# Optimization experiments

Hardware: AMD Instinct MI355X
Metric: run time of the kernel (lower is better)

Reference implementation:

```python
import jax, jax.numpy as jnp
import numpy as np

EPS = 1e-12  # torch F.normalize eps

def _l2norm(v, axis):
    n = jnp.linalg.norm(v, axis=axis, keepdims=True)
    return v / jnp.maximum(n, EPS)

def setup_inputs() -> dict:
    key = jax.random.key(0)
    k1, k2, k3 = jax.random.split(key, 3)
    N, D, H, W, K = 32, 512, 40, 40, 64
    x = jax.random.normal(k1, (N, D, H, W), dtype=jnp.float32)
    conv_weight = jax.random.normal(k2, (K, D), dtype=jnp.float32) * 0.05
    centroids = jax.random.uniform(k3, (K, D), dtype=jnp.float32)
    return {"x": x, "conv_weight": conv_weight, "centroids": centroids}

def reference(x, conv_weight, centroids):
    N, D, H, W = x.shape
    K = centroids.shape[0]
    # descriptor-wise L2 normalization over channel dim
    x = _l2norm(x, axis=1)
    x_flat = x.reshape(N, D, H * W)                       # [N, D, S]
    # 1x1 conv == per-pixel linear: [K,D] @ [N,D,S] -> [N,K,S]
    logits = jnp.einsum('kd,nds->nks', conv_weight, x_flat)
    soft_assign = jax.nn.softmax(logits, axis=1)          # softmax over clusters
    # vlad[n,k,d] = sum_s a[n,k,s] * (x[n,d,s] - c[k,d])
    #            = (a @ x^T) - (sum_s a) * c   -- two GEMM-like ops, no K-loop
    agg = jnp.einsum('nks,nds->nkd', soft_assign, x_flat)  # [N, K, D]
    a_sum = soft_assign.sum(axis=2)                        # [N, K]
    vlad = agg - a_sum[:, :, None] * centroids[None, :, :]
    # intra-normalization over D, flatten, global L2 normalization
    vlad = _l2norm(vlad, axis=2)
    vlad = vlad.reshape(N, K * D)
    vlad = _l2norm(vlad, axis=1)
    return vlad
```

## Files before the change

### kernel.cpp

```cpp
#include <hip/hip_runtime.h>
#include <math.h>

#define N_ 32
#define D_ 512
#define S_ 1600
#define K_ 64

#define APL 72

typedef __attribute__((ext_vector_type(8))) short short8;
typedef __attribute__((ext_vector_type(4))) float f32x4;
typedef __attribute__((ext_vector_type(2))) unsigned u32x2;

static __device__ __forceinline__ short f2bf(float f) {
    unsigned u = __float_as_uint(f);
    u += 0x7fffu + ((u >> 16) & 1u);
    return (short)(u >> 16);
}
static __device__ __forceinline__ unsigned pk2(float a, float b) {
    return (unsigned)(unsigned short)f2bf(a) | ((unsigned)(unsigned short)f2bf(b) << 16);
}

__global__ __launch_bounds__(256) void kW(const float* __restrict__ w,
                                          short* __restrict__ w16)
{
    int i4 = (blockIdx.x * 256 + threadIdx.x) * 4;
    float4 v = *(const float4*)&w[i4];
    short4 h = {f2bf(v.x), f2bf(v.y), f2bf(v.z), f2bf(v.w)};
    *(short4*)&w16[i4] = h;
}

__global__ __launch_bounds__(256) void kA(const float* __restrict__ x,
                                          const short* __restrict__ w16,
                                          short* __restrict__ aprime,
                                          float* __restrict__ asum)
{
    __shared__ short T[64 * 512];
    __shared__ short aPl[64 * APL];
    __shared__ float invSS[64];
    __shared__ float invL[64];
    __shared__ float wredS[4][66];

    const int tid = threadIdx.x;
    const int wv  = tid >> 6;
    const int l   = tid & 63;
    const int lk  = l & 15;
    const int q   = l >> 4;
    const int n   = blockIdx.x / 25;
    const int s0  = (blockIdx.x % 25) * 64;

    const float* xb = x + (size_t)n * D_ * S_;

    const int sT     = 4 * lk + q;
    const int sTbase = sT * 512;
    const int smask  = (sT & 7) << 3;
    const int rmask  = (lk & 7) << 3;

    if (tid < 64) invSS[tid] = 0.f;
    __syncthreads();

    float ssql[4] = {0.f, 0.f, 0.f, 0.f};
#pragma unroll
    for (int j = 0; j < 32; ++j) {
        const int d = 16 * j + 4 * wv + q;
        const float4 v = *(const float4*)&xb[(size_t)d * S_ + s0 + 4 * lk];
        ssql[0] += v.x * v.x;  ssql[1] += v.y * v.y;
        ssql[2] += v.z * v.z;  ssql[3] += v.w * v.w;
        unsigned p0 = pk2(v.x, v.y), p1 = pk2(v.z, v.w);
        unsigned mine = (l & 32) ? p0 : p1;
        unsigned oth  = (unsigned)__shfl_xor((int)mine, 32);
        unsigned a0 = (l & 32) ? oth : p0;
        unsigned a1 = (l & 32) ? p1 : oth;
        unsigned r0 = (unsigned)__shfl_xor((int)a0, 16);
        unsigned r1 = (unsigned)__shfl_xor((int)a1, 16);
        unsigned o0, o1;
        if (l & 16) {
            o0 = (r0 >> 16) | (a0 & 0xffff0000u);
            o1 = (r1 >> 16) | (a1 & 0xffff0000u);
        } else {
            o0 = (a0 & 0xffffu) | (r0 << 16);
            o1 = (a1 & 0xffffu) | (r1 << 16);
        }
        *(u32x2*)&T[sTbase + ((16 * j + 4 * wv) ^ smask)] = (u32x2){o0, o1};
    }
#pragma unroll
    for (int i = 0; i < 4; ++i) atomicAdd(&invSS[4 * lk + i], ssql[i]);
    __syncthreads();

    if (tid < 64) invL[tid] = 1.0f / fmaxf(sqrtf(invSS[tid]), 1e-12f);

    f32x4 accl[4];
#pragma unroll
    for (int st = 0; st < 4; ++st) accl[st] = (f32x4){0.f, 0.f, 0.f, 0.f};
    const short* wrow = w16 + (size_t)(16 * wv + lk) * D_;
#pragma unroll
    for (int kst = 0; kst < 16; ++kst) {
        short8 af = *(const short8*)&wrow[kst * 32 + q * 8];
        const int off = (kst * 32 + q * 8) ^ rmask;
#pragma unroll
        for (int st = 0; st < 4; ++st) {
            short8 b = *(const short8*)&T[(st * 16 + lk) * 512 + off];
            accl[st] = __builtin_amdgcn_mfma_f32_16x16x32_bf16(af, b, accl[st], 0, 0, 0);
        }
    }
    __syncthreads();

    float e[4][4], invv[4];
#pragma unroll
    for (int st = 0; st < 4; ++st) {
        invv[st] = invL[st * 16 + lk];
        float sm = 0.f;
#pragma unroll
        for (int r = 0; r < 4; ++r) {
            e[st][r] = __expf(accl[st][r] * invv[st]);
            sm += e[st][r];
        }
        sm += __shfl_xor(sm, 16);
        sm += __shfl_xor(sm, 32);
        if (q == 0) wredS[wv][st * 16 + lk] = sm;
    }
    __syncthreads();

    float asum_loc[4] = {0.f, 0.f, 0.f, 0.f};
#pragma unroll
    for (int st = 0; st < 4; ++st) {
        const int s = st * 16 + lk;
        const float rs = 1.0f / (wredS[0][s] + wredS[1][s]
                               + wredS[2][s] + wredS[3][s]);
#pragma unroll
        for (int r = 0; r < 4; ++r) {
            const float p = e[st][r] * rs;
            aPl[(16 * wv + 4 * q + r) * APL + s] = f2bf(p * invv[st]);
            asum_loc[r] += p;
        }
    }
    __syncthreads();

    {
        const int kk = tid >> 2;
        const int c0 = (tid & 3) * 16;
        short8 w0 = *(const short8*)&aPl[kk * APL + c0];
        short8 w1 = *(const short8*)&aPl[kk * APL + c0 + 8];
        short* apb = aprime + (size_t)n * K_ * S_ + (size_t)kk * S_ + s0 + c0;
        *(short8*)apb       = w0;
        *(short8*)(apb + 8) = w1;
    }

#pragma unroll
    for (int r = 0; r < 4; ++r) {
        float v = asum_loc[r];
        v += __shfl_xor(v, 1);  v += __shfl_xor(v, 2);
        v += __shfl_xor(v, 4);  v += __shfl_xor(v, 8);
        if (lk == 0) atomicAdd(&asum[n * K_ + 16 * wv + 4 * q + r], v);
    }
}

__global__ __launch_bounds__(256) void kB(const float* __restrict__ x,
                                          const short* __restrict__ aprime,
                                          float* __restrict__ agg)
{
    const int bid = blockIdx.x;
    const int n  = bid / 20;
    const int dt = (bid % 20) / 5;
    const int sp = bid % 5;
    const int wv = threadIdx.x >> 6;
    const int l  = threadIdx.x & 63;
    const int lk = l & 15;
    const int q  = l >> 4;
    const int dbase = dt * 128 + wv * 32;

    const short* ap = aprime + (size_t)n * K_ * S_;
    const float* xb = x + (size_t)n * D_ * S_;

    f32x4 acc[4][2];
#pragma unroll
    for (int kt = 0; kt < 4; ++kt)
#pragma unroll
        for (int ds = 0; ds < 2; ++ds) acc[kt][ds] = (f32x4){0.f, 0.f, 0.f, 0.f};

    for (int kst = 0; kst < 10; ++kst) {
        const int s = sp * 320 + kst * 32 + q * 8;
        short8 af[4];
#pragma unroll
        for (int kt = 0; kt < 4; ++kt)
            af[kt] = *(const short8*)&ap[(size_t)(kt * 16 + lk) * S_ + s];
        short8 bf[2];
#pragma unroll
        for (int ds = 0; ds < 2; ++ds) {
            const float* xp = &xb[(size_t)(dbase + ds * 16 + lk) * S_ + s];
            float4 v0 = *(const float4*)xp;
            float4 v1 = *(const float4*)(xp + 4);
            short8 b;
            b[0] = f2bf(v0.x); b[1] = f2bf(v0.y); b[2] = f2bf(v0.z); b[3] = f2bf(v0.w);
            b[4] = f2bf(v1.x); b[5] = f2bf(v1.y); b[6] = f2bf(v1.z); b[7] = f2bf(v1.w);
            bf[ds] = b;
        }
#pragma unroll
        for (int kt = 0; kt < 4; ++kt)
#pragma unroll
            for (int ds = 0; ds < 2; ++ds)
                acc[kt][ds] = __builtin_amdgcn_mfma_f32_16x16x32_bf16(af[kt], bf[ds], acc[kt][ds], 0, 0, 0);
    }

    float* ab = agg + (size_t)n * K_ * D_;
#pragma unroll
    for (int kt = 0; kt < 4; ++kt)
#pragma unroll
        for (int ds = 0; ds < 2; ++ds)
#pragma unroll
            for (int r = 0; r < 4; ++r)
                atomicAdd(&ab[(size_t)(kt * 16 + 4 * q + r) * D_ + dbase + ds * 16 + lk],
                          acc[kt][ds][r]);
}

__global__ __launch_bounds__(256) void kC(const float* __restrict__ agg,
                                          const float* __restrict__ asum,
                                          const float* __restrict__ cent,
                                          float* __restrict__ out)
{
    __shared__ float red[4];
    const int tid = threadIdx.x;
    const int nk = blockIdx.x;
    const int k = nk & 63;
    const float as = asum[nk];
    const float* cb = cent + (size_t)k * D_;
    const float* ag = agg + (size_t)nk * D_;

    float v0 = ag[tid]       - as * cb[tid];
    float v1 = ag[tid + 256] - as * cb[tid + 256];
    float ssq = v0 * v0 + v1 * v1;

    ssq += __shfl_xor(ssq, 32);
    ssq += __shfl_xor(ssq, 16);
    ssq += __shfl_xor(ssq, 8);
    ssq += __shfl_xor(ssq, 4);
    ssq += __shfl_xor(ssq, 2);
    ssq += __shfl_xor(ssq, 1);
    if ((tid & 63) == 0) red[tid >> 6] = ssq;
    __syncthreads();
    const float total = red[0] + red[1] + red[2] + red[3];
    const float scale = 1.0f / (fmaxf(sqrtf(total), 1e-12f) * 8.0f);

    out[(size_t)nk * D_ + tid]       = v0 * scale;
    out[(size_t)nk * D_ + tid + 256] = v1 * scale;
}

extern "C" void kernel_launch(void* const* d_in, const int* in_sizes, int n_in,
                              void* d_out, int out_size, void* d_ws, size_t ws_size,
                              hipStream_t stream)
{
    const float* x    = (const float*)d_in[0];
    const float* w    = (const float*)d_in[1];
    const float* cent = (const float*)d_in[2];
    float* out = (float*)d_out;

    float* agg    = (float*)d_ws;
    float* asum   = agg + (size_t)N_ * K_ * D_;
    short* aprime = (short*)(asum + N_ * K_);
    short* w16    = aprime + (size_t)N_ * K_ * S_;

    hipMemsetAsync(agg, 0, ((size_t)N_ * K_ * D_ + N_ * K_) * sizeof(float), stream);

    kW<<<32, 256, 0, stream>>>(w, w16);
    kA<<<N_ * (S_ / 64), 256, 0, stream>>>(x, w16, aprime, asum);
    kB<<<N_ * 4 * 5, 256, 0, stream>>>(x, aprime, agg);
    kC<<<N_ * K_, 256, 0, stream>>>(agg, asum, cent, out);
}
```

Baseline: 232.5 us.

## Rewrite assignment kernel as single-wave blocks loading x directly into MFMA fragments

The soft-assignment kernel changes from 256-thread blocks that stage a 64-pixel tile of x into LDS (with shuffle transposes and several barriers) to 64-thread single-wave blocks that each own 16 pixels. Each wave reads x columns straight from global memory into bf16 B fragments, computes all 64 clusters, and does the norm and softmax reductions with wave shuffles only. This removes the LDS staging, atomics and barriers, and gives four times as many blocks. In exchange, global loads become scalar strided 4-byte reads (16 consecutive floats per row, i.e. 64-byte segments), the aprime stores are uncoalesced 2-byte writes, and there are more asum atomics.

Result: faster. 222.2 us (-4.5%).

```diff
diff --git a/kernel.cpp b/kernel.cpp
--- a/kernel.cpp
+++ b/kernel.cpp
@@ -6,20 +6,14 @@
 #define S_ 1600
 #define K_ 64
 
-#define APL 72
-
 typedef __attribute__((ext_vector_type(8))) short short8;
 typedef __attribute__((ext_vector_type(4))) float f32x4;
-typedef __attribute__((ext_vector_type(2))) unsigned u32x2;
 
 static __device__ __forceinline__ short f2bf(float f) {
     unsigned u = __float_as_uint(f);
     u += 0x7fffu + ((u >> 16) & 1u);
     return (short)(u >> 16);
 }
-static __device__ __forceinline__ unsigned pk2(float a, float b) {
-    return (unsigned)(unsigned short)f2bf(a) | ((unsigned)(unsigned short)f2bf(b) << 16);
-}
 
 __global__ __launch_bounds__(256) void kW(const float* __restrict__ w,
                                           short* __restrict__ w16)
@@ -30,129 +24,74 @@
     *(short4*)&w16[i4] = h;
 }
 
-__global__ __launch_bounds__(256) void kA(const float* __restrict__ x,
-                                          const short* __restrict__ w16,
-                                          short* __restrict__ aprime,
-                                          float* __restrict__ asum)
-{
-    __shared__ short T[64 * 512];
-    __shared__ short aPl[64 * APL];
-    __shared__ float invSS[64];
-    __shared__ float invL[64];
-    __shared__ float wredS[4][66];
-
-    const int tid = threadIdx.x;
-    const int wv  = tid >> 6;
-    const int l   = tid & 63;
+__global__ __launch_bounds__(64) void kA(const float* __restrict__ x,
+                                         const short* __restrict__ w16,
+                                         short* __restrict__ aprime,
+                                         float* __restrict__ asum)
+{
+    const int l   = threadIdx.x;
     const int lk  = l & 15;
     const int q   = l >> 4;
-    const int n   = blockIdx.x / 25;
-    const int s0  = (blockIdx.x % 25) * 64;
-
-    const float* xb = x + (size_t)n * D_ * S_;
-
-    const int sT     = 4 * lk + q;
-    const int sTbase = sT * 512;
-    const int smask  = (sT & 7) << 3;
-    const int rmask  = (lk & 7) << 3;
-
-    if (tid < 64) invSS[tid] = 0.f;
-    __syncthreads();
-
-    float ssql[4] = {0.f, 0.f, 0.f, 0.f};
-#pragma unroll
-    for (int j = 0; j < 32; ++j) {
-        const int d = 16 * j + 4 * wv + q;
-        const float4 v = *(const float4*)&xb[(size_t)d * S_ + s0 + 4 * lk];
-        ssql[0] += v.x * v.x;  ssql[1] += v.y * v.y;
-        ssql[2] += v.z * v.z;  ssql[3] += v.w * v.w;
-        unsigned p0 = pk2(v.x, v.y), p1 = pk2(v.z, v.w);
-        unsigned mine = (l & 32) ? p0 : p1;
-        unsigned oth  = (unsigned)__shfl_xor((int)mine, 32);
-        unsigned a0 = (l & 32) ? oth : p0;
-        unsigned a1 = (l & 32) ? p1 : oth;
-        unsigned r0 = (unsigned)__shfl_xor((int)a0, 16);
-        unsigned r1 = (unsigned)__shfl_xor((int)a1, 16);
-        unsigned o0, o1;
-        if (l & 16) {
-            o0 = (r0 >> 16) | (a0 & 0xffff0000u);
-            o1 = (r1 >> 16) | (a1 & 0xffff0000u);
-        } else {
-            o0 = (a0 & 0xffffu) | (r0 << 16);
-            o1 = (a1 & 0xffffu) | (r1 << 16);
-        }
-        *(u32x2*)&T[sTbase + ((16 * j + 4 * wv) ^ smask)] = (u32x2){o0, o1};
+    const int n   = blockIdx.x / 100;
+    const int s0w = (blockIdx.x % 100) * 16;
+
+    const float* xcol = x + (size_t)n * D_ * S_ + s0w + lk;
+
+    f32x4 accl[4];
+#pragma unroll
+    for (int kt = 0; kt < 4; ++kt) accl[kt] = (f32x4){0.f, 0.f, 0.f, 0.f};
+    float ssq = 0.f;
+
+#pragma unroll 2
+    for (int kst = 0; kst < 16; ++kst) {
+        float xv[8];
+#pragma unroll
+        for (int j = 0; j < 8; ++j)
+            xv[j] = xcol[(size_t)(kst * 32 + q * 8 + j) * S_];
+        short8 bf;
+#pragma unroll
+        for (int j = 0; j < 8; ++j) {
+            ssq += xv[j] * xv[j];
+            bf[j] = f2bf(xv[j]);
+        }
+#pragma unroll
+        for (int kt = 0; kt < 4; ++kt) {
+            short8 af = *(const short8*)&w16[(size_t)(kt * 16 + lk) * D_ + kst * 32 + q * 8];
+            accl[kt] = __builtin_amdgcn_mfma_f32_16x16x32_bf16(af, bf, accl[kt], 0, 0, 0);
+        }
     }
-#pragma unroll
-    for (int i = 0; i < 4; ++i) atomicAdd(&invSS[4 * lk + i], ssql[i]);
-    __syncthreads();
-
-    if (tid < 64) invL[tid] = 1.0f / fmaxf(sqrtf(invSS[tid]), 1e-12f);
-
-    f32x4 accl[4];
-#pragma unroll
-    for (int st = 0; st < 4; ++st) accl[st] = (f32x4){0.f, 0.f, 0.f, 0.f};
-    const short* wrow = w16 + (size_t)(16 * wv + lk) * D_;
-#pragma unroll
-    for (int kst = 0; kst < 16; ++kst) {
-        short8 af = *(const short8*)&wrow[kst * 32 + q * 8];
-        const int off = (kst * 32 + q * 8) ^ rmask;
-#pragma unroll
-        for (int st = 0; st < 4; ++st) {
-            short8 b = *(const short8*)&T[(st * 16 + lk) * 512 + off];
-            accl[st] = __builtin_amdgcn_mfma_f32_16x16x32_bf16(af, b, accl[st], 0, 0, 0);
-        }
-    }
-    __syncthreads();
-
-    float e[4][4], invv[4];
-#pragma unroll
-    for (int st = 0; st < 4; ++st) {
-        invv[st] = invL[st * 16 + lk];
-        float sm = 0.f;
+
+    ssq += __shfl_xor(ssq, 16);
+    ssq += __shfl_xor(ssq, 32);
+    const float inv = 1.0f / fmaxf(sqrtf(ssq), 1e-12f);
+
+    float e[4][4];
+    float sm = 0.f;
+#pragma unroll
+    for (int kt = 0; kt < 4; ++kt)
 #pragma unroll
         for (int r = 0; r < 4; ++r) {
-            e[st][r] = __expf(accl[st][r] * invv[st]);
-            sm += e[st][r];
-        }
-        sm += __shfl_xor(sm, 16);
-        sm += __shfl_xor(sm, 32);
-        if (q == 0) wredS[wv][st * 16 + lk] = sm;
-    }
-    __syncthreads();
-
-    float asum_loc[4] = {0.f, 0.f, 0.f, 0.f};
-#pragma unroll
-    for (int st = 0; st < 4; ++st) {
-        const int s = st * 16 + lk;
-        const float rs = 1.0f / (wredS[0][s] + wredS[1][s]
-                               + wredS[2][s] + wredS[3][s]);
+            e[kt][r] = __expf(accl[kt][r] * inv);
+            sm += e[kt][r];
+        }
+    sm += __shfl_xor(sm, 16);
+    sm += __shfl_xor(sm, 32);
+    const float rs = 1.0f / sm;
+
+    short* apb = aprime + (size_t)n * K_ * S_ + s0w + lk;
+#pragma unroll
+    for (int kt = 0; kt < 4; ++kt)
 #pragma unroll
         for (int r = 0; r < 4; ++r) {
-            const float p = e[st][r] * rs;
-            aPl[(16 * wv + 4 * q + r) * APL + s] = f2bf(p * invv[st]);
-            asum_loc[r] += p;
-        }
-    }
-    __syncthreads();
-
-    {
-        const int kk = tid >> 2;
-        const int c0 = (tid & 3) * 16;
-        short8 w0 = *(const short8*)&aPl[kk * APL + c0];
-        short8 w1 = *(const short8*)&aPl[kk * APL + c0 + 8];
-        short* apb = aprime + (size_t)n * K_ * S_ + (size_t)kk * S_ + s0 + c0;
-        *(short8*)apb       = w0;
-        *(short8*)(apb + 8) = w1;
-    }
-
-#pragma unroll
-    for (int r = 0; r < 4; ++r) {
-        float v = asum_loc[r];
-        v += __shfl_xor(v, 1);  v += __shfl_xor(v, 2);
-        v += __shfl_xor(v, 4);  v += __shfl_xor(v, 8);
-        if (lk == 0) atomicAdd(&asum[n * K_ + 16 * wv + 4 * q + r], v);
-    }
+            const float p = e[kt][r] * rs;
+            apb[(size_t)(kt * 16 + 4 * q + r) * S_] = f2bf(p * inv);
+            float v = p;
+            v += __shfl_xor(v, 1);
+            v += __shfl_xor(v, 2);
+            v += __shfl_xor(v, 4);
+            v += __shfl_xor(v, 8);
+            if (lk == 0) atomicAdd(&asum[n * K_ + kt * 16 + 4 * q + r], v);
+        }
 }
 
 __global__ __launch_bounds__(256) void kB(const float* __restrict__ x,
@@ -262,7 +201,7 @@
     hipMemsetAsync(agg, 0, ((size_t)N_ * K_ * D_ + N_ * K_) * sizeof(float), stream);
 
     kW<<<32, 256, 0, stream>>>(w, w16);
-    kA<<<N_ * (S_ / 64), 256, 0, stream>>>(x, w16, aprime, asum);
+    kA<<<N_ * (S_ / 16), 64, 0, stream>>>(x, w16, aprime, asum);
     kB<<<N_ * 4 * 5, 256, 0, stream>>>(x, aprime, agg);
     kC<<<N_ * K_, 256, 0, stream>>>(agg, asum, cent, out);
 }
```

## Double-buffer kA over D chunks with small LDS, and split kB S-range finer

Applied to the files above, without the earlier changes.

kA no longer stages the full 64x512 bf16 tile of x in LDS. It processes D in eight chunks of 64 with a double-buffered 2x64x64 tile, so global loads of the next chunk overlap the MFMAs on the current one, and LDS use drops enough to allow more blocks per CU. The staging of the assignment matrix through LDS is removed: each thread writes its bf16 values straight to global memory as scattered 2-byte stores. kB now splits S into 10 parts instead of 5, doubling the grid and halving the loop length, which means twice as many atomic adds into agg.

Result: faster. 219.9 us (-5.4%).

```diff
diff --git a/kernel.cpp b/kernel.cpp
--- a/kernel.cpp
+++ b/kernel.cpp
@@ -6,9 +6,8 @@
 #define S_ 1600
 #define K_ 64
 
-#define APL 72
-
 typedef __attribute__((ext_vector_type(8))) short short8;
+typedef __attribute__((ext_vector_type(4))) short short4v;
 typedef __attribute__((ext_vector_type(4))) float f32x4;
 typedef __attribute__((ext_vector_type(2))) unsigned u32x2;
 
@@ -35,10 +34,8 @@
                                           short* __restrict__ aprime,
                                           float* __restrict__ asum)
 {
-    __shared__ short T[64 * 512];
-    __shared__ short aPl[64 * APL];
+    __shared__ short T[2][64 * 64];
     __shared__ float invSS[64];
-    __shared__ float invL[64];
     __shared__ float wredS[4][66];
 
     const int tid = threadIdx.x;
@@ -50,65 +47,88 @@
     const int s0  = (blockIdx.x % 25) * 64;
 
     const float* xb = x + (size_t)n * D_ * S_;
-
-    const int sT     = 4 * lk + q;
-    const int sTbase = sT * 512;
-    const int smask  = (sT & 7) << 3;
-    const int rmask  = (lk & 7) << 3;
+    const float* xrow = xb + (size_t)(4 * wv + q) * S_ + s0 + 4 * lk;
+    const int row   = 4 * lk + q;
+    const int rswz  = row & 15;
+
+    float ssql[4] = {0.f, 0.f, 0.f, 0.f};
+    f32x4 accl[4];
+#pragma unroll
+    for (int st = 0; st < 4; ++st) accl[st] = (f32x4){0.f, 0.f, 0.f, 0.f};
 
     if (tid < 64) invSS[tid] = 0.f;
+
+#define STAGE(c, b)                                                          \
+    {                                                                        \
+        float4 v[4];                                                         \
+        _Pragma("unroll")                                                    \
+        for (int jj = 0; jj < 4; ++jj)                                       \
+            v[jj] = *(const float4*)&xrow[(size_t)(64 * (c) + 16 * jj) * S_];\
+        _Pragma("unroll")                                                    \
+        for (int jj = 0; jj < 4; ++jj) {                                     \
+            ssql[0] += v[jj].x * v[jj].x;  ssql[1] += v[jj].y * v[jj].y;     \
+            ssql[2] += v[jj].z * v[jj].z;  ssql[3] += v[jj].w * v[jj].w;     \
+            unsigned p0 = pk2(v[jj].x, v[jj].y), p1 = pk2(v[jj].z, v[jj].w); \
+            unsigned mine = (l & 32) ? p0 : p1;                              \
+            unsigned oth  = (unsigned)__shfl_xor((int)mine, 32);             \
+            unsigned a0 = (l & 32) ? oth : p0;                               \
+            unsigned a1 = (l & 32) ? p1 : oth;                               \
+            unsigned r0 = (unsigned)__shfl_xor((int)a0, 16);                 \
+            unsigned r1 = (unsigned)__shfl_xor((int)a1, 16);                 \
+            unsigned o0, o1;                                                 \
+            if (l & 16) {                                                    \
+                o0 = (r0 >> 16) | (a0 & 0xffff0000u);                        \
+                o1 = (r1 >> 16) | (a1 & 0xffff0000u);                        \
+            } else {                                                         \
+                o0 = (a0 & 0xffffu) | (r0 << 16);                            \
+                o1 = (a1 & 0xffffu) | (r1 << 16);                            \
+            }                                                                \
+            *(u32x2*)&T[b][row * 64 + (((4 * jj + wv) ^ rswz) << 2)] =       \
+                (u32x2){o0, o1};                                             \
+        }                                                                    \
+    }
+
+    STAGE(0, 0);
     __syncthreads();
 
-    float ssql[4] = {0.f, 0.f, 0.f, 0.f};
-#pragma unroll
-    for (int j = 0; j < 32; ++j) {
-        const int d = 16 * j + 4 * wv + q;
-        const float4 v = *(const float4*)&xb[(size_t)d * S_ + s0 + 4 * lk];
-        ssql[0] += v.x * v.x;  ssql[1] += v.y * v.y;
-        ssql[2] += v.z * v.z;  ssql[3] += v.w * v.w;
-        unsigned p0 = pk2(v.x, v.y), p1 = pk2(v.z, v.w);
-        unsigned mine = (l & 32) ? p0 : p1;
-        unsigned oth  = (unsigned)__shfl_xor((int)mine, 32);
-        unsigned a0 = (l & 32) ? oth : p0;
-        unsigned a1 = (l & 32) ? p1 : oth;
-        unsigned r0 = (unsigned)__shfl_xor((int)a0, 16);
-        unsigned r1 = (unsigned)__shfl_xor((int)a1, 16);
-        unsigned o0, o1;
-        if (l & 16) {
-            o0 = (r0 >> 16) | (a0 & 0xffff0000u);
-            o1 = (r1 >> 16) | (a1 & 0xffff0000u);
-        } else {
-            o0 = (a0 & 0xffffu) | (r0 << 16);
-            o1 = (a1 & 0xffffu) | (r1 << 16);
-        }
-        *(u32x2*)&T[sTbase + ((16 * j + 4 * wv) ^ smask)] = (u32x2){o0, o1};
-    }
-#pragma unroll
-    for (int i = 0; i < 4; ++i) atomicAdd(&invSS[4 * lk + i], ssql[i]);
-    __syncthreads();
-
-    if (tid < 64) invL[tid] = 1.0f / fmaxf(sqrtf(invSS[tid]), 1e-12f);
-
-    f32x4 accl[4];
-#pragma unroll
-    for (int st = 0; st < 4; ++st) accl[st] = (f32x4){0.f, 0.f, 0.f, 0.f};
-    const short* wrow = w16 + (size_t)(16 * wv + lk) * D_;
-#pragma unroll
-    for (int kst = 0; kst < 16; ++kst) {
-        short8 af = *(const short8*)&wrow[kst * 32 + q * 8];
-        const int off = (kst * 32 + q * 8) ^ rmask;
-#pragma unroll
-        for (int st = 0; st < 4; ++st) {
-            short8 b = *(const short8*)&T[(st * 16 + lk) * 512 + off];
-            accl[st] = __builtin_amdgcn_mfma_f32_16x16x32_bf16(af, b, accl[st], 0, 0, 0);
-        }
-    }
-    __syncthreads();
+    for (int c = 0; c < 8; ++c) {
+        if (c < 7) {
+            if ((c & 1) == 0) STAGE(c + 1, 1) else STAGE(c + 1, 0)
+        }
+        const int b = c & 1;
+#pragma unroll
+        for (int kl = 0; kl < 2; ++kl) {
+            short8 af = *(const short8*)&w16[(size_t)(16 * wv + lk) * D_
+                                             + 64 * c + 32 * kl + 8 * q];
+#pragma unroll
+            for (int st = 0; st < 4; ++st) {
+                const int rr = st * 16 + lk;
+                const int c4 = 8 * kl + 2 * q;
+                short4v pa = *(const short4v*)&T[b][rr * 64 + (((c4    ) ^ (rr & 15)) << 2)];
+                short4v pb = *(const short4v*)&T[b][rr * 64 + (((c4 + 1) ^ (rr & 15)) << 2)];
+                short8 bf = {pa[0], pa[1], pa[2], pa[3], pb[0], pb[1], pb[2], pb[3]};
+                accl[st] = __builtin_amdgcn_mfma_f32_16x16x32_bf16(af, bf, accl[st], 0, 0, 0);
+            }
+        }
+        if (c == 7) {
+#pragma unroll
+            for (int i = 0; i < 4; ++i) {
+                ssql[i] += __shfl_xor(ssql[i], 16);
+                ssql[i] += __shfl_xor(ssql[i], 32);
+            }
+            if (q == 0) {
+#pragma unroll
+                for (int i = 0; i < 4; ++i) atomicAdd(&invSS[4 * lk + i], ssql[i]);
+            }
+        }
+        __syncthreads();
+    }
+#undef STAGE
 
     float e[4][4], invv[4];
 #pragma unroll
     for (int st = 0; st < 4; ++st) {
-        invv[st] = invL[st * 16 + lk];
+        invv[st] = 1.0f / fmaxf(sqrtf(invSS[st * 16 + lk]), 1e-12f);
         float sm = 0.f;
 #pragma unroll
         for (int r = 0; r < 4; ++r) {
@@ -122,6 +142,7 @@
     __syncthreads();
 
     float asum_loc[4] = {0.f, 0.f, 0.f, 0.f};
+    short* apb = aprime + (size_t)n * K_ * S_ + s0;
 #pragma unroll
     for (int st = 0; st < 4; ++st) {
         const int s = st * 16 + lk;
@@ -130,22 +151,10 @@
 #pragma unroll
         for (int r = 0; r < 4; ++r) {
             const float p = e[st][r] * rs;
-            aPl[(16 * wv + 4 * q + r) * APL + s] = f2bf(p * invv[st]);
+            apb[(size_t)(16 * wv + 4 * q + r) * S_ + s] = f2bf(p * invv[st]);
             asum_loc[r] += p;
         }
     }
-    __syncthreads();
-
-    {
-        const int kk = tid >> 2;
-        const int c0 = (tid & 3) * 16;
-        short8 w0 = *(const short8*)&aPl[kk * APL + c0];
-        short8 w1 = *(const short8*)&aPl[kk * APL + c0 + 8];
-        short* apb = aprime + (size_t)n * K_ * S_ + (size_t)kk * S_ + s0 + c0;
-        *(short8*)apb       = w0;
-        *(short8*)(apb + 8) = w1;
-    }
-
 #pragma unroll
     for (int r = 0; r < 4; ++r) {
         float v = asum_loc[r];
@@ -160,9 +169,9 @@
                                           float* __restrict__ agg)
 {
     const int bid = blockIdx.x;
-    const int n  = bid / 20;
-    const int dt = (bid % 20) / 5;
-    const int sp = bid % 5;
+    const int n  = bid / 40;
+    const int dt = (bid % 40) / 10;
+    const int sp = bid % 10;
     const int wv = threadIdx.x >> 6;
     const int l  = threadIdx.x & 63;
     const int lk = l & 15;
@@ -178,8 +187,9 @@
 #pragma unroll
         for (int ds = 0; ds < 2; ++ds) acc[kt][ds] = (f32x4){0.f, 0.f, 0.f, 0.f};
 
-    for (int kst = 0; kst < 10; ++kst) {
-        const int s = sp * 320 + kst * 32 + q * 8;
+#pragma unroll
+    for (int kst = 0; kst < 5; ++kst) {
+        const int s = sp * 160 + kst * 32 + q * 8;
         short8 af[4];
 #pragma unroll
         for (int kt = 0; kt < 4; ++kt)
@@ -263,6 +273,6 @@
 
     kW<<<32, 256, 0, stream>>>(w, w16);
     kA<<<N_ * (S_ / 64), 256, 0, stream>>>(x, w16, aprime, asum);
-    kB<<<N_ * 4 * 5, 256, 0, stream>>>(x, aprime, agg);
+    kB<<<N_ * 4 * 10, 256, 0, stream>>>(x, aprime, agg);
     kC<<<N_ * K_, 256, 0, stream>>>(agg, asum, cent, out);
 }
```
